# Kernel optimization log

Hardware: AMD Instinct MI355X
Metric: run time of the kernel (lower is better)

The kernel has to match this reference:

```python
import jax, jax.numpy as jnp
import numpy as np

N = 20000   # nodes
E = 100000  # edges per relation
R = 4       # relations
H = 4       # heads
D = 64      # embed_dim (per-head dim == embed_dim in this module)
F = 128     # node_feat_dim
L = 2       # layers
EPS = 1e-5  # torch LayerNorm default


def setup_inputs() -> dict:
    key = jax.random.key(0)
    ks = jax.random.split(key, 32)
    s = 0.05
    inp = {}
    inp["nodes"] = jnp.arange(N)
    inp["node_features"] = jax.random.normal(ks[0], (N, F), jnp.float32)
    inp["betweenness"] = jax.random.uniform(ks[1], (N,), jnp.float32)
    inp["closeness"] = jax.random.uniform(ks[2], (N,), jnp.float32)
    inp["node_sign_influence"] = jax.random.normal(ks[3], (N,), jnp.float32)
    inp["edge_src"] = jax.random.randint(ks[4], (R, E), 0, N)
    inp["edge_tgt"] = jax.random.randint(ks[5], (R, E), 0, N)
    # encoder params
    inp["enc_Wf"] = jax.random.normal(ks[6], (F, D), jnp.float32) * s
    inp["enc_bf"] = jnp.full((D,), 0.01, jnp.float32)
    inp["enc_Wc"] = jax.random.normal(ks[7], (2, D), jnp.float32) * s
    inp["enc_bc"] = jnp.full((D,), 0.01, jnp.float32)
    # per-layer, per-relation attention params
    inp["Wq"] = jax.random.normal(ks[8], (L, R, D, D * H), jnp.float32) * s
    inp["bq"] = jnp.zeros((L, R, D * H), jnp.float32)
    inp["Wk"] = jax.random.normal(ks[9], (L, R, D, D * H), jnp.float32) * s
    inp["bk"] = jnp.zeros((L, R, D * H), jnp.float32)
    inp["Wv"] = jax.random.normal(ks[10], (L, R, D, D * H), jnp.float32) * s
    inp["bv"] = jnp.zeros((L, R, D * H), jnp.float32)
    inp["Wp"] = jax.random.normal(ks[11], (L, R * H * D, D), jnp.float32) * s
    inp["bp"] = jnp.zeros((L, D), jnp.float32)
    inp["sign_w"] = jax.random.normal(ks[12], (L, H, R), jnp.float32) * s
    inp["ln_g"] = jnp.ones((L, D), jnp.float32)
    inp["ln_b"] = jnp.zeros((L, D), jnp.float32)
    return inp


def reference(nodes, node_features, betweenness, closeness, node_sign_influence,
              edge_src, edge_tgt, enc_Wf, enc_bf, enc_Wc, enc_bc,
              Wq, bq, Wk, bk, Wv, bv, Wp, bp, sign_w, ln_g, ln_b):
    # CentralityAwareEncoder
    cen = jnp.stack([betweenness[nodes], closeness[nodes]], axis=1)  # [N, 2]
    x = node_features[nodes] @ enc_Wf + enc_bf + cen @ enc_Wc + enc_bc  # [N, D]
    n = x.shape[0]
    inv_sqrt_d = 1.0 / jnp.sqrt(jnp.float32(D))
    for l in range(L):  # structural loop over layers
        outs = []
        for r in range(R):  # structural loop over relations
            src, tgt = edge_src[r], edge_tgt[r]
            Q = (x @ Wq[l, r] + bq[l, r]).reshape(n, H, D)
            K = (x @ Wk[l, r] + bk[l, r]).reshape(n, H, D)
            V = (x @ Wv[l, r] + bv[l, r]).reshape(n, H, D)
            # edge-wise scores [E, H]
            scores = jnp.einsum('ehd,ehd->eh', Q[src], K[tgt]) * inv_sqrt_d
            scores = scores * (node_sign_influence[src][:, None] * sign_w[l, :, r][None, :])
            # segment softmax over src (all heads at once)
            mx = jax.ops.segment_max(scores, src, num_segments=n)
            ex = jnp.exp(scores - mx[src])
            den = jax.ops.segment_sum(ex, src, num_segments=n)
            attn = ex / (den[src] + 1e-10)  # [E, H]  (dropout: eval mode, identity)
            wV = V[tgt] * attn[..., None]   # [E, H, D]
            out = jax.ops.segment_sum(wV, src, num_segments=n)  # [N, H, D]
            outs.append(out.reshape(n, H * D))
        attn_out = jnp.concatenate(outs, axis=-1) @ Wp[l] + bp[l]  # [N, D]
        y = x + attn_out
        mu = y.mean(-1, keepdims=True)
        var = y.var(-1, keepdims=True)
        x = (y - mu) * jax.lax.rsqrt(var + EPS) * ln_g[l] + ln_b[l]
    return x
```

## Files before the change

kernel.cpp:

```cpp
#include <hip/hip_runtime.h>
#include <math.h>

#define NN 20000
#define EE 100000
#define RR 4
#define HH 4
#define DD 64
#define FF 128
#define LL 2

typedef __attribute__((ext_vector_type(8))) short bf16x8;
typedef __attribute__((ext_vector_type(4))) float f32x4;

__device__ __forceinline__ ushort f2bf(float f) {
  uint u = __float_as_uint(f);
  u += 0x7FFFu + ((u >> 16) & 1u);
  return (ushort)(u >> 16);
}
__device__ __forceinline__ float bf2f(ushort h) {
  return __uint_as_float((uint)h << 16);
}

__global__ __launch_bounds__(256) void enc_prep_kernel(
    const float* __restrict__ feat, const float* __restrict__ bet,
    const float* __restrict__ clo, const float* __restrict__ Wf,
    const float* __restrict__ bf, const float* __restrict__ Wc,
    const float* __restrict__ bc, float* __restrict__ x,
    ushort* __restrict__ xbf, const float* __restrict__ Wq,
    const float* __restrict__ bq, const float* __restrict__ Wk,
    const float* __restrict__ bk, const float* __restrict__ Wv,
    const float* __restrict__ bv, const float* __restrict__ Wp,
    ushort* __restrict__ mT, ushort* __restrict__ gT, float* __restrict__ cvec,
    float* __restrict__ gam) {
  const int t = threadIdx.x;
  if (blockIdx.x < 5000) {
    __shared__ float fs[4][FF];
    const int n0 = blockIdx.x * 4;
    for (int idx = t; idx < 4 * FF; idx += 256) {
      const int rr = idx >> 7, cc = idx & 127;
      const int n = n0 + rr;
      fs[rr][cc] = (n < NN) ? feat[(size_t)n * FF + cc] : 0.f;
    }
    __syncthreads();
    const int g = t >> 6, d = t & 63;
    const int n = n0 + g;
    if (n >= NN) return;
    float acc = bf[d] + bc[d] + bet[n] * Wc[d] + clo[n] * Wc[DD + d];
#pragma unroll 8
    for (int f = 0; f < FF; ++f) acc = fmaf(fs[g][f], Wf[f * DD + d], acc);
    x[(size_t)n * DD + d] = acc;
    xbf[(size_t)n * DD + d] = f2bf(acc);
    return;
  }
  const int idx = (blockIdx.x - 5000) * 256 + t;
  const int R1 = LL * RR * 272 * 64;
  const int R2 = LL * 64 * 1024;
  if (idx < R1) {
    const int lr = idx / (272 * 64);
    const int rem = idx % (272 * 64);
    const int col = rem >> 6, i = rem & 63;
    const float* wq = Wq + (size_t)lr * 64 * 256;
    const float* wk = Wk + (size_t)lr * 64 * 256;
    float v = 0.f;
    if (col < 256) {
      const int h = col >> 6, j = col & 63;
      const float* qa = wq + (size_t)i * 256 + h * 64;
      const float* kb = wk + (size_t)j * 256 + h * 64;
#pragma unroll 8
      for (int d = 0; d < 64; ++d) v = fmaf(qa[d], kb[d], v);
    } else if (col < 260) {
      const int h = col - 256;
      const float* qa = wq + (size_t)i * 256 + h * 64;
      const float* bb = bk + lr * 256 + h * 64;
#pragma unroll 8
      for (int d = 0; d < 64; ++d) v = fmaf(qa[d], bb[d], v);
    } else if (col < 264) {
      const int h = col - 260;
      const float* ka = wk + (size_t)i * 256 + h * 64;
      const float* bb = bq + lr * 256 + h * 64;
#pragma unroll 8
      for (int d = 0; d < 64; ++d) v = fmaf(ka[d], bb[d], v);
    }
    mT[idx] = f2bf(v);
  } else if (idx < R1 + R2) {
    const int id = idx - R1;
    const int lj = id >> 10;
    const int k = id & 1023;
    const int l = lj >> 6, j = lj & 63;
    const int r = k >> 8, h = (k >> 6) & 3, v_ = k & 63;
    const float* wv =
        Wv + (size_t)(l * RR + r) * 64 * 256 + (size_t)v_ * 256 + h * 64;
    const float* wp =
        Wp + (size_t)l * 65536 + (size_t)(r * 256 + h * 64) * 64 + j;
    float s = 0.f;
#pragma unroll 8
    for (int d = 0; d < 64; ++d) s = fmaf(wv[d], wp[d * 64], s);
    gT[id] = f2bf(s);
  } else if (idx < R1 + R2 + 512) {
    const int id = idx - R1 - R2;
    const int l = id >> 8, rj = id & 255;
    const int r = rj >> 6, j = rj & 63;
    const float* bb = bv + (l * RR + r) * 256;
    const float* wp = Wp + (size_t)l * 65536 + (size_t)(r * 256) * 64 + j;
    float s = 0.f;
    for (int q2 = 0; q2 < 256; ++q2) s = fmaf(bb[q2], wp[q2 * 64], s);
    cvec[id] = s;
  } else if (idx < R1 + R2 + 512 + 32) {
    const int id = idx - R1 - R2 - 512;
    const int lr = id >> 2, h = id & 3;
    const float* a = bq + lr * 256 + h * 64;
    const float* b2 = bk + lr * 256 + h * 64;
    float s = 0.f;
    for (int d = 0; d < 64; ++d) s = fmaf(a[d], b2[d], s);
    gam[id] = s;
  }
}

__global__ __launch_bounds__(256) void hist_kernel(
    const int* __restrict__ esrc, int* __restrict__ counts) {
  const int e = blockIdx.x * 256 + threadIdx.x;
  const int r = blockIdx.y;
  if (e < EE) atomicAdd(&counts[r * NN + esrc[(size_t)r * EE + e]], 1);
}

__global__ __launch_bounds__(1024) void scan_kernel(
    const int* __restrict__ counts, int* __restrict__ offs) {
  __shared__ int ts[1024];
  const int r = blockIdx.x, t = threadIdx.x;
  const int base = t * 20;
  int loc[20];
  int run = 0;
#pragma unroll
  for (int k = 0; k < 20; ++k) {
    const int i = base + k;
    const int v = (i < NN) ? counts[r * NN + i] : 0;
    run += v;
    loc[k] = run;
  }
  ts[t] = run;
  __syncthreads();
#pragma unroll
  for (int s = 1; s < 1024; s <<= 1) {
    const int add = (t >= s) ? ts[t - s] : 0;
    __syncthreads();
    ts[t] += add;
    __syncthreads();
  }
  const int prev = (t == 0) ? 0 : ts[t - 1];
#pragma unroll
  for (int k = 0; k < 20; ++k) {
    const int i = base + k;
    if (i < NN) offs[r * (NN + 1) + i + 1] = prev + loc[k];
  }
  if (t == 0) offs[r * (NN + 1)] = 0;
}

__global__ __launch_bounds__(256) void fill_kernel(
    const int* __restrict__ esrc, const int* __restrict__ etgt,
    const int* __restrict__ offs, int* __restrict__ cursor,
    int* __restrict__ csr) {
  const int e = blockIdx.x * 256 + threadIdx.x;
  const int r = blockIdx.y;
  if (e < EE) {
    const int s = esrc[(size_t)r * EE + e];
    const int pos = offs[r * (NN + 1) + s] + atomicAdd(&cursor[r * NN + s], 1);
    csr[(size_t)r * EE + pos] = etgt[(size_t)r * EE + e];
  }
}

__global__ __launch_bounds__(256) void yattn_kernel(
    const ushort* __restrict__ xbf, const int* __restrict__ offs4,
    const int* __restrict__ csr4, const float* __restrict__ nsi,
    const float* __restrict__ sw_l, const float* __restrict__ gam_l,
    const ushort* __restrict__ mT_l, const ushort* __restrict__ gT,
    float* __restrict__ partial) {
  __shared__ ushort ys[16][264];
  __shared__ float alph[16][4];
  const int t = threadIdx.x;
  const int w = t >> 6, l = t & 63;
  const int hi = l >> 4, lo = l & 15;
  const int h = hi;
  const int m0 = blockIdx.x * 16;
  const int r = blockIdx.y;
  const ushort* mTr = mT_l + (size_t)r * 17408;

  const ushort* arow = xbf + (size_t)(m0 + lo) * 64 + hi * 8;
  const bf16x8 a0 = *(const bf16x8*)(arow);
  const bf16x8 a1 = *(const bf16x8*)(arow + 32);
#pragma unroll
  for (int nt = 0; nt < 4; ++nt) {
    const int col0 = w * 64 + nt * 16;
    const ushort* brow = mTr + (size_t)(col0 + lo) * 64 + hi * 8;
    const bf16x8 b0 = *(const bf16x8*)(brow);
    const bf16x8 b1 = *(const bf16x8*)(brow + 32);
    f32x4 z = {0.f, 0.f, 0.f, 0.f};
    z = __builtin_amdgcn_mfma_f32_16x16x32_bf16(a0, b0, z, 0, 0, 0);
    z = __builtin_amdgcn_mfma_f32_16x16x32_bf16(a1, b1, z, 0, 0, 0);
    const int col = col0 + lo;
    const float wb = bf2f(mTr[(size_t)(260 + (col >> 6)) * 64 + (col & 63)]);
#pragma unroll
    for (int i = 0; i < 4; ++i) {
      ys[hi * 4 + i][col] = f2bf(z[i] + wb);
    }
  }
  if (w == 3) {
    const ushort* brow = mTr + (size_t)(256 + lo) * 64 + hi * 8;
    const bf16x8 b0 = *(const bf16x8*)(brow);
    const bf16x8 b1 = *(const bf16x8*)(brow + 32);
    f32x4 z = {0.f, 0.f, 0.f, 0.f};
    z = __builtin_amdgcn_mfma_f32_16x16x32_bf16(a0, b0, z, 0, 0, 0);
    z = __builtin_amdgcn_mfma_f32_16x16x32_bf16(a1, b1, z, 0, 0, 0);
    if (lo < 4) {
#pragma unroll
      for (int i = 0; i < 4; ++i) alph[hi * 4 + i][lo] = z[i];
    }
  }
  __syncthreads();

  const int* offs = offs4 + r * (NN + 1);
  const int* csr = csr4 + (size_t)r * EE;
  const float swh = sw_l[h * RR + r];
  const float gamh = gam_l[r * 4 + h];
#pragma unroll
  for (int k = 0; k < 4; ++k) {
    const int idx = w * 4 + k;
    const int n = m0 + idx;
    const ushort4 yu = *(const ushort4*)&ys[idx][l * 4];
    const float y0 = bf2f(yu.x), y1 = bf2f(yu.y), y2 = bf2f(yu.z),
                y3 = bf2f(yu.w);
    const float c2 = 0.18033688f * nsi[n] * swh;
    const float ac2 = (alph[idx][h] + gamh) * c2;
    const int s0 = offs[n], e0 = offs[n + 1];
    float denA = 0.f, oA0 = 0.f, oA1 = 0.f, oA2 = 0.f, oA3 = 0.f;
    float denB = 0.f, oB0 = 0.f, oB1 = 0.f, oB2 = 0.f, oB3 = 0.f;
    int i = s0;
    for (; i + 1 < e0; i += 2) {
      const int tgA = __builtin_amdgcn_readfirstlane(csr[i]);
      const int tgB = __builtin_amdgcn_readfirstlane(csr[i + 1]);
      const ushort4 cxA = *(const ushort4*)(xbf + (size_t)tgA * 64 + lo * 4);
      const ushort4 cxB = *(const ushort4*)(xbf + (size_t)tgB * 64 + lo * 4);
      const float xA0 = bf2f(cxA.x), xA1 = bf2f(cxA.y), xA2 = bf2f(cxA.z),
                  xA3 = bf2f(cxA.w);
      const float xB0 = bf2f(cxB.x), xB1 = bf2f(cxB.y), xB2 = bf2f(cxB.z),
                  xB3 = bf2f(cxB.w);
      float dA = y0 * xA0;
      float dB = y0 * xB0;
      dA = fmaf(y1, xA1, dA);
      dB = fmaf(y1, xB1, dB);
      dA = fmaf(y2, xA2, dA);
      dB = fmaf(y2, xB2, dB);
      dA = fmaf(y3, xA3, dA);
      dB = fmaf(y3, xB3, dB);
#pragma unroll
      for (int dd = 1; dd < 16; dd <<= 1) {
        dA += __shfl_xor(dA, dd);
        dB += __shfl_xor(dB, dd);
      }
      const float ewA = __builtin_amdgcn_exp2f(fmaf(dA, c2, ac2));
      const float ewB = __builtin_amdgcn_exp2f(fmaf(dB, c2, ac2));
      denA += ewA;
      denB += ewB;
      oA0 = fmaf(ewA, xA0, oA0);
      oB0 = fmaf(ewB, xB0, oB0);
      oA1 = fmaf(ewA, xA1, oA1);
      oB1 = fmaf(ewB, xB1, oB1);
      oA2 = fmaf(ewA, xA2, oA2);
      oB2 = fmaf(ewB, xB2, oB2);
      oA3 = fmaf(ewA, xA3, oA3);
      oB3 = fmaf(ewB, xB3, oB3);
    }
    if (i < e0) {
      const int tg = __builtin_amdgcn_readfirstlane(csr[i]);
      const ushort4 cx = *(const ushort4*)(xbf + (size_t)tg * 64 + lo * 4);
      const float x0 = bf2f(cx.x), x1 = bf2f(cx.y), x2 = bf2f(cx.z),
                  x3 = bf2f(cx.w);
      float d = y0 * x0;
      d = fmaf(y1, x1, d);
      d = fmaf(y2, x2, d);
      d = fmaf(y3, x3, d);
#pragma unroll
      for (int dd = 1; dd < 16; dd <<= 1) d += __shfl_xor(d, dd);
      const float ew = __builtin_amdgcn_exp2f(fmaf(d, c2, ac2));
      denA += ew;
      oA0 = fmaf(ew, x0, oA0);
      oA1 = fmaf(ew, x1, oA1);
      oA2 = fmaf(ew, x2, oA2);
      oA3 = fmaf(ew, x3, oA3);
    }
    const float inv = 1.f / (denA + denB + 1e-10f);
    ushort4 ou;
    ou.x = f2bf((oA0 + oB0) * inv);
    ou.y = f2bf((oA1 + oB1) * inv);
    ou.z = f2bf((oA2 + oB2) * inv);
    ou.w = f2bf((oA3 + oB3) * inv);
    *(ushort4*)&ys[idx][l * 4] = ou;
  }
  __syncthreads();

  f32x4 acc = {0.f, 0.f, 0.f, 0.f};
#pragma unroll
  for (int ks = 0; ks < 8; ++ks) {
    const bf16x8 a = *(const bf16x8*)&ys[lo][ks * 32 + hi * 8];
    const bf16x8 bb = *(const bf16x8*)(gT + (size_t)(w * 16 + lo) * 1024 +
                                       r * 256 + ks * 32 + hi * 8);
    acc = __builtin_amdgcn_mfma_f32_16x16x32_bf16(a, bb, acc, 0, 0, 0);
  }
#pragma unroll
  for (int i = 0; i < 4; ++i) {
    partial[((size_t)r * NN + m0 + hi * 4 + i) * 64 + w * 16 + lo] = acc[i];
  }
}

__global__ __launch_bounds__(256) void ln_kernel(
    const float* __restrict__ partial, const float* __restrict__ xin,
    const float* __restrict__ bp, const float* __restrict__ g,
    const float* __restrict__ b, const int* __restrict__ offs4,
    const float* __restrict__ cvec_l, float* __restrict__ xout,
    ushort* __restrict__ xbf_out) {
  const int t = threadIdx.x;
  const int w = t >> 6, l = t & 63;
  const int m0 = blockIdx.x * 16;
#pragma unroll
  for (int k = 0; k < 4; ++k) {
    const int n = m0 + w * 4 + k;
    float v = partial[((size_t)0 * NN + n) * 64 + l] +
              partial[((size_t)1 * NN + n) * 64 + l] +
              partial[((size_t)2 * NN + n) * 64 + l] +
              partial[((size_t)3 * NN + n) * 64 + l];
#pragma unroll
    for (int r = 0; r < 4; ++r) {
      const bool nz = offs4[r * (NN + 1) + n + 1] > offs4[r * (NN + 1) + n];
      v += nz ? cvec_l[r * 64 + l] : 0.f;
    }
    const float y = v + bp[l] + xin[(size_t)n * 64 + l];
    float s = y, s2 = y * y;
#pragma unroll
    for (int dd = 1; dd < 64; dd <<= 1) {
      s += __shfl_xor(s, dd);
      s2 += __shfl_xor(s2, dd);
    }
    const float mu = s * (1.f / 64.f);
    const float var = s2 * (1.f / 64.f) - mu * mu;
    const float xo = (y - mu) * rsqrtf(var + 1e-5f) * g[l] + b[l];
    xout[(size_t)n * 64 + l] = xo;
    if (xbf_out) xbf_out[(size_t)n * 64 + l] = f2bf(xo);
  }
}

extern "C" void kernel_launch(void* const* d_in, const int* in_sizes, int n_in,
                              void* d_out, int out_size, void* d_ws,
                              size_t ws_size, hipStream_t stream) {
  const float* feat = (const float*)d_in[1];
  const float* bet = (const float*)d_in[2];
  const float* clo = (const float*)d_in[3];
  const float* nsi = (const float*)d_in[4];
  const int* esrc = (const int*)d_in[5];
  const int* etgt = (const int*)d_in[6];
  const float* Wf = (const float*)d_in[7];
  const float* bf = (const float*)d_in[8];
  const float* Wc = (const float*)d_in[9];
  const float* bc = (const float*)d_in[10];
  const float* Wq = (const float*)d_in[11];
  const float* bq = (const float*)d_in[12];
  const float* Wk = (const float*)d_in[13];
  const float* bk = (const float*)d_in[14];
  const float* Wv = (const float*)d_in[15];
  const float* bv = (const float*)d_in[16];
  const float* Wp = (const float*)d_in[17];
  const float* bp = (const float*)d_in[18];
  const float* sw = (const float*)d_in[19];
  const float* lng = (const float*)d_in[20];
  const float* lnb = (const float*)d_in[21];
  float* out = (float*)d_out;

  char* base = (char*)d_ws;
  size_t off = 0;
  auto alloc = [&](size_t bytes) {
    void* p = base + off;
    off += (bytes + 255) & ~(size_t)255;
    return p;
  };
  float* xa = (float*)alloc((size_t)NN * DD * 4);
  float* xb = (float*)alloc((size_t)NN * DD * 4);
  ushort* xbf = (ushort*)alloc((size_t)NN * DD * 2);
  float* partial = (float*)alloc((size_t)RR * NN * 64 * 4);
  ushort* mT = (ushort*)alloc((size_t)LL * RR * 272 * 64 * 2);
  ushort* gT = (ushort*)alloc((size_t)LL * 64 * 1024 * 2);
  float* cvec = (float*)alloc((size_t)LL * RR * 64 * 4);
  float* gam = (float*)alloc((size_t)LL * RR * HH * 4);
  int* counts = (int*)alloc((size_t)RR * NN * 4);
  int* offsb = (int*)alloc((size_t)RR * (NN + 1) * 4);
  int* csr = (int*)alloc((size_t)RR * EE * 4);
  (void)ws_size;

  hipMemsetAsync(counts, 0, (size_t)RR * NN * 4, stream);
  {
    dim3 gg((EE + 255) / 256, RR);
    hipLaunchKernelGGL(hist_kernel, gg, dim3(256), 0, stream, esrc, counts);
  }
  hipLaunchKernelGGL(scan_kernel, dim3(RR), dim3(1024), 0, stream, counts,
                     offsb);
  hipMemsetAsync(counts, 0, (size_t)RR * NN * 4, stream);
  {
    dim3 gg((EE + 255) / 256, RR);
    hipLaunchKernelGGL(fill_kernel, gg, dim3(256), 0, stream, esrc, etgt, offsb,
                       counts, csr);
  }

  hipLaunchKernelGGL(enc_prep_kernel, dim3(6059), dim3(256), 0, stream, feat,
                     bet, clo, Wf, bf, Wc, bc, xa, xbf, Wq, bq, Wk, bk, Wv, bv,
                     Wp, mT, gT, cvec, gam);

  for (int l = 0; l < LL; ++l) {
    const float* xin = (l == 0) ? xa : xb;
    float* xout = (l == LL - 1) ? out : xb;
    ushort* xbf_next = (l == LL - 1) ? (ushort*)nullptr : xbf;
    hipLaunchKernelGGL(yattn_kernel, dim3(NN / 16, RR), dim3(256), 0, stream,
                       xbf, offsb, csr, nsi, sw + l * HH * RR, gam + l * 16,
                       mT + (size_t)l * RR * 17408, gT + (size_t)l * 65536,
                       partial);
    hipLaunchKernelGGL(ln_kernel, dim3(NN / 16), dim3(256), 0, stream, partial,
                       xin, bp + l * 64, lng + l * 64, lnb + l * 64, offsb,
                       cvec + l * 256, xout, xbf_next);
  }
}
```

Before: 278.6 us.

## Fold histogram into encoder kernel, reset counts in scan, double yattn row tile

The edge histogram now runs as extra blocks of the encoder/prep kernel, and the scan kernel zeroes the counts it reads, so one kernel launch and one memset are removed. The attention kernel now handles 32 nodes per block instead of 16. This reuses the loaded weight fragments across two MFMA row tiles and prefetches the gT fragments into registers before the barrier. Risks are higher register and LDS use per block, and half as many blocks, which reduces parallelism for the irregular per-node edge loops.

```diff
diff --git a/kernel.cpp b/kernel.cpp
--- a/kernel.cpp
+++ b/kernel.cpp
@@ -31,8 +31,17 @@
     const float* __restrict__ bk, const float* __restrict__ Wv,
     const float* __restrict__ bv, const float* __restrict__ Wp,
     ushort* __restrict__ mT, ushort* __restrict__ gT, float* __restrict__ cvec,
-    float* __restrict__ gam) {
+    float* __restrict__ gam, const int* __restrict__ esrc,
+    int* __restrict__ counts) {
   const int t = threadIdx.x;
+  if (blockIdx.x >= 6059) {
+    const int gid = (blockIdx.x - 6059) * 256 + t;
+    if (gid < RR * EE) {
+      const int r = gid / EE;
+      atomicAdd(&counts[r * NN + esrc[gid]], 1);
+    }
+    return;
+  }
   if (blockIdx.x < 5000) {
     __shared__ float fs[4][FF];
     const int n0 = blockIdx.x * 4;
@@ -116,15 +125,8 @@
   }
 }
 
-__global__ __launch_bounds__(256) void hist_kernel(
-    const int* __restrict__ esrc, int* __restrict__ counts) {
-  const int e = blockIdx.x * 256 + threadIdx.x;
-  const int r = blockIdx.y;
-  if (e < EE) atomicAdd(&counts[r * NN + esrc[(size_t)r * EE + e]], 1);
-}
-
 __global__ __launch_bounds__(1024) void scan_kernel(
-    const int* __restrict__ counts, int* __restrict__ offs) {
+    int* __restrict__ counts, int* __restrict__ offs) {
   __shared__ int ts[1024];
   const int r = blockIdx.x, t = threadIdx.x;
   const int base = t * 20;
@@ -134,6 +136,7 @@
   for (int k = 0; k < 20; ++k) {
     const int i = base + k;
     const int v = (i < NN) ? counts[r * NN + i] : 0;
+    if (i < NN) counts[r * NN + i] = 0;
     run += v;
     loc[k] = run;
   }
@@ -174,45 +177,58 @@
     const float* __restrict__ sw_l, const float* __restrict__ gam_l,
     const ushort* __restrict__ mT_l, const ushort* __restrict__ gT,
     float* __restrict__ partial) {
-  __shared__ ushort ys[16][264];
-  __shared__ float alph[16][4];
+  __shared__ ushort ys[32][264];
+  __shared__ float alph[32][4];
   const int t = threadIdx.x;
   const int w = t >> 6, l = t & 63;
   const int hi = l >> 4, lo = l & 15;
   const int h = hi;
-  const int m0 = blockIdx.x * 16;
+  const int m0 = blockIdx.x * 32;
   const int r = blockIdx.y;
   const ushort* mTr = mT_l + (size_t)r * 17408;
 
-  const ushort* arow = xbf + (size_t)(m0 + lo) * 64 + hi * 8;
-  const bf16x8 a0 = *(const bf16x8*)(arow);
-  const bf16x8 a1 = *(const bf16x8*)(arow + 32);
+  const ushort* arow0 = xbf + (size_t)(m0 + lo) * 64 + hi * 8;
+  const ushort* arow1 = xbf + (size_t)(m0 + 16 + lo) * 64 + hi * 8;
+  const bf16x8 a00 = *(const bf16x8*)(arow0);
+  const bf16x8 a01 = *(const bf16x8*)(arow0 + 32);
+  const bf16x8 a10 = *(const bf16x8*)(arow1);
+  const bf16x8 a11 = *(const bf16x8*)(arow1 + 32);
 #pragma unroll
   for (int nt = 0; nt < 4; ++nt) {
     const int col0 = w * 64 + nt * 16;
     const ushort* brow = mTr + (size_t)(col0 + lo) * 64 + hi * 8;
     const bf16x8 b0 = *(const bf16x8*)(brow);
     const bf16x8 b1 = *(const bf16x8*)(brow + 32);
-    f32x4 z = {0.f, 0.f, 0.f, 0.f};
-    z = __builtin_amdgcn_mfma_f32_16x16x32_bf16(a0, b0, z, 0, 0, 0);
-    z = __builtin_amdgcn_mfma_f32_16x16x32_bf16(a1, b1, z, 0, 0, 0);
+    f32x4 z0 = {0.f, 0.f, 0.f, 0.f};
+    z0 = __builtin_amdgcn_mfma_f32_16x16x32_bf16(a00, b0, z0, 0, 0, 0);
+    z0 = __builtin_amdgcn_mfma_f32_16x16x32_bf16(a01, b1, z0, 0, 0, 0);
+    f32x4 z1 = {0.f, 0.f, 0.f, 0.f};
+    z1 = __builtin_amdgcn_mfma_f32_16x16x32_bf16(a10, b0, z1, 0, 0, 0);
+    z1 = __builtin_amdgcn_mfma_f32_16x16x32_bf16(a11, b1, z1, 0, 0, 0);
     const int col = col0 + lo;
     const float wb = bf2f(mTr[(size_t)(260 + (col >> 6)) * 64 + (col & 63)]);
 #pragma unroll
     for (int i = 0; i < 4; ++i) {
-      ys[hi * 4 + i][col] = f2bf(z[i] + wb);
+      ys[hi * 4 + i][col] = f2bf(z0[i] + wb);
+      ys[16 + hi * 4 + i][col] = f2bf(z1[i] + wb);
     }
   }
   if (w == 3) {
     const ushort* brow = mTr + (size_t)(256 + lo) * 64 + hi * 8;
     const bf16x8 b0 = *(const bf16x8*)(brow);
     const bf16x8 b1 = *(const bf16x8*)(brow + 32);
-    f32x4 z = {0.f, 0.f, 0.f, 0.f};
-    z = __builtin_amdgcn_mfma_f32_16x16x32_bf16(a0, b0, z, 0, 0, 0);
-    z = __builtin_amdgcn_mfma_f32_16x16x32_bf16(a1, b1, z, 0, 0, 0);
+    f32x4 z0 = {0.f, 0.f, 0.f, 0.f};
+    z0 = __builtin_amdgcn_mfma_f32_16x16x32_bf16(a00, b0, z0, 0, 0, 0);
+    z0 = __builtin_amdgcn_mfma_f32_16x16x32_bf16(a01, b1, z0, 0, 0, 0);
+    f32x4 z1 = {0.f, 0.f, 0.f, 0.f};
+    z1 = __builtin_amdgcn_mfma_f32_16x16x32_bf16(a10, b0, z1, 0, 0, 0);
+    z1 = __builtin_amdgcn_mfma_f32_16x16x32_bf16(a11, b1, z1, 0, 0, 0);
     if (lo < 4) {
 #pragma unroll
-      for (int i = 0; i < 4; ++i) alph[hi * 4 + i][lo] = z[i];
+      for (int i = 0; i < 4; ++i) {
+        alph[hi * 4 + i][lo] = z0[i];
+        alph[16 + hi * 4 + i][lo] = z1[i];
+      }
     }
   }
   __syncthreads();
@@ -221,9 +237,8 @@
   const int* csr = csr4 + (size_t)r * EE;
   const float swh = sw_l[h * RR + r];
   const float gamh = gam_l[r * 4 + h];
-#pragma unroll
-  for (int k = 0; k < 4; ++k) {
-    const int idx = w * 4 + k;
+  for (int k = 0; k < 8; ++k) {
+    const int idx = w * 8 + k;
     const int n = m0 + idx;
     const ushort4 yu = *(const ushort4*)&ys[idx][l * 4];
     const float y0 = bf2f(yu.x), y1 = bf2f(yu.y), y2 = bf2f(yu.z),
@@ -295,19 +310,29 @@
     ou.w = f2bf((oA3 + oB3) * inv);
     *(ushort4*)&ys[idx][l * 4] = ou;
   }
+
+  bf16x8 gb[8];
+#pragma unroll
+  for (int ks = 0; ks < 8; ++ks) {
+    gb[ks] = *(const bf16x8*)(gT + (size_t)(w * 16 + lo) * 1024 + r * 256 +
+                              ks * 32 + hi * 8);
+  }
   __syncthreads();
 
-  f32x4 acc = {0.f, 0.f, 0.f, 0.f};
+  f32x4 acc0 = {0.f, 0.f, 0.f, 0.f};
+  f32x4 acc1 = {0.f, 0.f, 0.f, 0.f};
 #pragma unroll
   for (int ks = 0; ks < 8; ++ks) {
-    const bf16x8 a = *(const bf16x8*)&ys[lo][ks * 32 + hi * 8];
-    const bf16x8 bb = *(const bf16x8*)(gT + (size_t)(w * 16 + lo) * 1024 +
-                                       r * 256 + ks * 32 + hi * 8);
-    acc = __builtin_amdgcn_mfma_f32_16x16x32_bf16(a, bb, acc, 0, 0, 0);
+    const bf16x8 aA = *(const bf16x8*)&ys[lo][ks * 32 + hi * 8];
+    const bf16x8 aB = *(const bf16x8*)&ys[16 + lo][ks * 32 + hi * 8];
+    acc0 = __builtin_amdgcn_mfma_f32_16x16x32_bf16(aA, gb[ks], acc0, 0, 0, 0);
+    acc1 = __builtin_amdgcn_mfma_f32_16x16x32_bf16(aB, gb[ks], acc1, 0, 0, 0);
   }
 #pragma unroll
   for (int i = 0; i < 4; ++i) {
-    partial[((size_t)r * NN + m0 + hi * 4 + i) * 64 + w * 16 + lo] = acc[i];
+    partial[((size_t)r * NN + m0 + hi * 4 + i) * 64 + w * 16 + lo] = acc0[i];
+    partial[((size_t)r * NN + m0 + 16 + hi * 4 + i) * 64 + w * 16 + lo] =
+        acc1[i];
   }
 }
 
@@ -394,28 +419,23 @@
   (void)ws_size;
 
   hipMemsetAsync(counts, 0, (size_t)RR * NN * 4, stream);
-  {
-    dim3 gg((EE + 255) / 256, RR);
-    hipLaunchKernelGGL(hist_kernel, gg, dim3(256), 0, stream, esrc, counts);
-  }
+  hipLaunchKernelGGL(enc_prep_kernel, dim3(6059 + (RR * EE + 255) / 256),
+                     dim3(256), 0, stream, feat, bet, clo, Wf, bf, Wc, bc, xa,
+                     xbf, Wq, bq, Wk, bk, Wv, bv, Wp, mT, gT, cvec, gam, esrc,
+                     counts);
   hipLaunchKernelGGL(scan_kernel, dim3(RR), dim3(1024), 0, stream, counts,
                      offsb);
-  hipMemsetAsync(counts, 0, (size_t)RR * NN * 4, stream);
   {
     dim3 gg((EE + 255) / 256, RR);
     hipLaunchKernelGGL(fill_kernel, gg, dim3(256), 0, stream, esrc, etgt, offsb,
                        counts, csr);
   }
 
-  hipLaunchKernelGGL(enc_prep_kernel, dim3(6059), dim3(256), 0, stream, feat,
-                     bet, clo, Wf, bf, Wc, bc, xa, xbf, Wq, bq, Wk, bk, Wv, bv,
-                     Wp, mT, gT, cvec, gam);
-
   for (int l = 0; l < LL; ++l) {
     const float* xin = (l == 0) ? xa : xb;
     float* xout = (l == LL - 1) ? out : xb;
     ushort* xbf_next = (l == LL - 1) ? (ushort*)nullptr : xbf;
-    hipLaunchKernelGGL(yattn_kernel, dim3(NN / 16, RR), dim3(256), 0, stream,
+    hipLaunchKernelGGL(yattn_kernel, dim3(NN / 32, RR), dim3(256), 0, stream,
                        xbf, offsb, csr, nsi, sw + l * HH * RR, gam + l * 16,
                        mT + (size_t)l * RR * 17408, gT + (size_t)l * 65536,
                        partial);
```

New measurement: 265.8 us. 4.6% less time.
